# Optimization experiments

Hardware: AMD Instinct MI355X
Metric: run time of the kernel (lower is better)

Reference implementation:

```python
import jax, jax.numpy as jnp
import numpy as np

N, E, IN, HID, ADIM, EDIM, H = 20000, 320000, 128, 128, 16, 16, 2


def _lin(key, out_d, in_d, scale=0.05):
    kw, kb = jax.random.split(key)
    W = jax.random.normal(kw, (out_d, in_d), jnp.float32) * scale
    b = jax.random.normal(kb, (out_d,), jnp.float32) * scale
    return W, b


def _gat_params(key):
    k = jax.random.split(key, 4)
    Wl, bl = _lin(k[0], H * HID, HID)
    Wr, br = _lin(k[1], H * HID, HID)
    We = jax.random.normal(k[2], (H * HID, EDIM), jnp.float32) * 0.05  # lin_edge, no bias
    att = jax.random.normal(k[3], (1, H, HID), jnp.float32) * 0.05
    bias = jnp.zeros((HID,), jnp.float32)  # concat=False -> out bias of size HID
    return Wl, bl, Wr, br, We, att, bias


def setup_inputs() -> dict:
    key = jax.random.key(0)
    ks = jax.random.split(key, 16)
    inp = {}
    inp['x'] = jax.random.normal(ks[0], (N, IN), jnp.float32)
    inp['edge_index'] = jax.random.randint(ks[1], (2, E), 0, N, jnp.int64 if jax.config.jax_enable_x64 else jnp.int32)
    inp['edge_attr'] = jax.random.normal(ks[2], (E, EDIM), jnp.float32)
    inp['action'] = jax.random.normal(ks[3], (N, ADIM), jnp.float32)
    inp['inp_W'], inp['inp_b'] = _lin(ks[4], HID, IN)
    for i, name in enumerate(['s1', 's2', 'sa']):
        Wl, bl, Wr, br, We, att, bias = _gat_params(ks[5 + i])
        inp[f'{name}_Wl'], inp[f'{name}_bl'] = Wl, bl
        inp[f'{name}_Wr'], inp[f'{name}_br'] = Wr, br
        inp[f'{name}_We'], inp[f'{name}_att'], inp[f'{name}_bias'] = We, att, bias
    inp['ap_W'], inp['ap_b'] = _lin(ks[8], HID, ADIM)
    inp['g_W'], inp['g_b'] = _lin(ks[9], HID, HID)
    inp['be_W'], inp['be_b'] = _lin(ks[10], HID, HID)
    inp['q1_W'], inp['q1_b'] = _lin(ks[11], HID, HID)
    inp['q2_W'], inp['q2_b'] = _lin(ks[12], 1, HID)
    return inp


def gatv2(h, src, dst, ea, Wl, bl, Wr, br, We, att, bias):
    """PyG GATv2Conv, heads=H, concat=False (mean over heads), with edge_attr."""
    n = h.shape[0]
    xl = (h @ Wl.T + bl).reshape(n, H, HID)   # source transform
    xr = (h @ Wr.T + br).reshape(n, H, HID)   # destination transform
    em = (ea @ We.T).reshape(-1, H, HID)      # [E,H,C]
    m = jax.nn.leaky_relu(xl[src] + xr[dst] + em, 0.2)   # [E,H,C]
    logit = (m * att).sum(-1)                 # [E,H]
    lmax = jax.ops.segment_max(logit, dst, num_segments=n)
    w = jnp.exp(logit - lmax[dst])
    den = jax.ops.segment_sum(w, dst, num_segments=n)
    alpha = w / den[dst]                      # segment softmax over incoming edges
    out = jax.ops.segment_sum(alpha[..., None] * xl[src], dst, num_segments=n)  # [n,H,C]
    return out.mean(axis=1) + bias


def reference(x, edge_index, edge_attr, action, inp_W, inp_b,
              s1_Wl, s1_bl, s1_Wr, s1_br, s1_We, s1_att, s1_bias,
              s2_Wl, s2_bl, s2_Wr, s2_br, s2_We, s2_att, s2_bias,
              sa_Wl, sa_bl, sa_Wr, sa_br, sa_We, sa_att, sa_bias,
              ap_W, ap_b, g_W, g_b, be_W, be_b, q1_W, q1_b, q2_W, q2_b):
    src, dst = edge_index[0], edge_index[1]
    h = jax.nn.relu(x @ inp_W.T + inp_b)
    h = jax.nn.relu(gatv2(h, src, dst, edge_attr, s1_Wl, s1_bl, s1_Wr, s1_br, s1_We, s1_att, s1_bias))
    h = jax.nn.relu(gatv2(h, src, dst, edge_attr, s2_Wl, s2_bl, s2_Wr, s2_br, s2_We, s2_att, s2_bias))
    a = jax.nn.relu(action @ ap_W.T + ap_b)
    h = (a @ g_W.T + g_b) * h + (a @ be_W.T + be_b)   # FiLM modulation
    h = jax.nn.relu(gatv2(h, src, dst, edge_attr, sa_Wl, sa_bl, sa_Wr, sa_br, sa_We, sa_att, sa_bias))
    h = jax.nn.relu(h @ q1_W.T + q1_b)
    q_node = h @ q2_W.T + q2_b                         # [N,1]
    return q_node.mean(axis=0, keepdims=True)          # [1,1]
```

## Files before the change

### kernel.cpp

```cpp
#include <hip/hip_runtime.h>
#include <hip/hip_bf16.h>


typedef __attribute__((ext_vector_type(8))) short bf16x8;
typedef __attribute__((ext_vector_type(4))) float f32x4;
typedef __attribute__((ext_vector_type(2))) float f32x2;

#define ZERO8 ((bf16x8){0, 0, 0, 0, 0, 0, 0, 0})

__device__ __forceinline__ unsigned short f2bf(float f) {
    union { float f; unsigned int i; } v; v.f = f;
    unsigned int x = v.i;
    x += 0x7fffu + ((x >> 16) & 1u);
    return (unsigned short)(x >> 16);
}
__device__ __forceinline__ unsigned char f2fp8(float f) {
    return (unsigned char)(__builtin_amdgcn_cvt_pk_fp8_f32(f, f, 0, false) & 0xFF);
}
__device__ __forceinline__ void wave_lds_fence() {
    __builtin_amdgcn_wave_barrier();
    asm volatile("s_waitcnt lgkmcnt(0)" ::: "memory");
    __builtin_amdgcn_wave_barrier();
}

#define MAXCVT 16
struct CvtDescs {
    const float* src[MAXCVT];
    unsigned short* dst[MAXCVT];
    int n4[MAXCVT];
    int cnt;
};
__global__ __launch_bounds__(256) void cvt_many_kernel(CvtDescs d) {
    const int tid = blockIdx.x * blockDim.x + threadIdx.x;
    const int stride = gridDim.x * blockDim.x;
    for (int e = 0; e < d.cnt; ++e) {
        const float4* s = (const float4*)d.src[e];
        ushort4* o = (ushort4*)d.dst[e];
        const int n = d.n4[e];
        for (int i = tid; i < n; i += stride) {
            float4 v = s[i];
            o[i] = make_ushort4(f2bf(v.x), f2bf(v.y), f2bf(v.z), f2bf(v.w));
        }
    }
}

__global__ void hist_kernel(const int* __restrict__ dst, int* __restrict__ deg, int n) {
    int i = blockIdx.x * blockDim.x + threadIdx.x;
    if (i < n) atomicAdd(&deg[dst[i]], 1);
}

__global__ __launch_bounds__(1024) void scan_kernel(const int* __restrict__ deg,
                                                    int* __restrict__ rowp,
                                                    int* __restrict__ cur, int n) {
    __shared__ int sums[1024];
    const int t = threadIdx.x;
    const int PER = 20;
    int base = t * PER;
    int local[PER];
    int run = 0;
#pragma unroll
    for (int i = 0; i < PER; ++i) {
        int v = (base + i < n) ? deg[base + i] : 0;
        local[i] = run; run += v;
    }
    sums[t] = run; __syncthreads();
    for (int off = 1; off < 1024; off <<= 1) {
        int v = (t >= off) ? sums[t - off] : 0;
        __syncthreads();
        sums[t] += v;
        __syncthreads();
    }
    int offs = (t > 0) ? sums[t - 1] : 0;
#pragma unroll
    for (int i = 0; i < PER; ++i) {
        int idx = base + i;
        if (idx < n) { int v = offs + local[i]; rowp[idx] = v; cur[idx] = v; }
    }
    if (t == 0) rowp[n] = sums[1023];
}

__global__ void scatter_kernel(const int* __restrict__ src, const int* __restrict__ dst,
                               int* __restrict__ cur, const float4* __restrict__ ea,
                               int* __restrict__ csrs, int* __restrict__ csrd,
                               ushort4* __restrict__ eacsr, int n) {
    int i = blockIdx.x * blockDim.x + threadIdx.x;
    if (i < n) {
        int d = dst[i];
        int p = atomicAdd(&cur[d], 1);
        csrs[p] = src[i];
        csrd[p] = d;
        const float4* er = ea + (size_t)i * 4;
        ushort4* eo = eacsr + (size_t)p * 4;
#pragma unroll
        for (int q = 0; q < 4; ++q) {
            float4 v = er[q];
            eo[q] = make_ushort4(f2bf(v.x), f2bf(v.y), f2bf(v.z), f2bf(v.w));
        }
    }
}

template <bool RELU, bool SPLIT, bool AF32>
__global__ __launch_bounds__(256) void gemm_mfma_kernel(
    const void* __restrict__ Ap, const unsigned short* __restrict__ W,
    const float* __restrict__ bias0, const float* __restrict__ bias1, int bsplit,
    unsigned short* __restrict__ Cbf, unsigned char* __restrict__ Cf8,
    int M, int N, int K) {
    __shared__ unsigned char ctile[SPLIT ? 128 * 64 : 64];
    const int t = threadIdx.x;
    const int wave = t >> 6, lane = t & 63;
    const int lo = lane & 15, quad = lane >> 4;
    const int m0 = blockIdx.y * 128 + wave * 32;
    const int n0 = blockIdx.x * 64;

    f32x4 acc[2][4];
#pragma unroll
    for (int i = 0; i < 2; ++i)
#pragma unroll
        for (int j = 0; j < 4; ++j) acc[i][j] = (f32x4){0.f, 0.f, 0.f, 0.f};

    for (int k0 = 0; k0 < K; k0 += 32) {
        bf16x8 af[2], bfr[4];
#pragma unroll
        for (int mi = 0; mi < 2; ++mi) {
            const int mb = m0 + mi * 16;
            if (mb >= M) { af[mi] = ZERO8; continue; }
            if (AF32) {
                const float* A = (const float*)Ap;
                float4 a0 = *(const float4*)(A + (size_t)(mb + lo) * K + k0 + quad * 8);
                float4 a1 = *(const float4*)(A + (size_t)(mb + lo) * K + k0 + quad * 8 + 4);
                bf16x8 f;
                f[0] = (short)f2bf(a0.x); f[1] = (short)f2bf(a0.y);
                f[2] = (short)f2bf(a0.z); f[3] = (short)f2bf(a0.w);
                f[4] = (short)f2bf(a1.x); f[5] = (short)f2bf(a1.y);
                f[6] = (short)f2bf(a1.z); f[7] = (short)f2bf(a1.w);
                af[mi] = f;
            } else {
                const unsigned short* A = (const unsigned short*)Ap;
                af[mi] = *(const bf16x8*)(A + (size_t)(mb + lo) * K + k0 + quad * 8);
            }
        }
#pragma unroll
        for (int ni = 0; ni < 4; ++ni)
            bfr[ni] = *(const bf16x8*)(W + (size_t)(n0 + ni * 16 + lo) * K + k0 + quad * 8);
#pragma unroll
        for (int mi = 0; mi < 2; ++mi)
#pragma unroll
            for (int ni = 0; ni < 4; ++ni)
                acc[mi][ni] = __builtin_amdgcn_mfma_f32_16x16x32_bf16(af[mi], bfr[ni], acc[mi][ni], 0, 0, 0);
    }

    float bn[4];
#pragma unroll
    for (int ni = 0; ni < 4; ++ni) {
        const int n = n0 + ni * 16 + lo;
        const float* bp = (n < bsplit) ? bias0 : bias1;
        const int bi = (n < bsplit) ? n : n - bsplit;
        bn[ni] = bp[bi];
    }
    if (SPLIT) {
#pragma unroll
        for (int mi = 0; mi < 2; ++mi) {
#pragma unroll
            for (int ni = 0; ni < 4; ++ni) {
                const int n = ni * 16 + lo;
#pragma unroll
                for (int r = 0; r < 4; ++r) {
                    float o = acc[mi][ni][r] + bn[ni];
                    if (RELU) o = fmaxf(o, 0.f);
                    ctile[(wave * 32 + mi * 16 + quad * 4 + r) * 64 + n] = f2fp8(o);
                }
            }
        }
        __syncthreads();
        const int row = t >> 1, half = t & 1;
        const int grow = blockIdx.y * 128 + row;
        if (grow < M) {
            const unsigned char* srcp = &ctile[row * 64 + half * 32];
            unsigned char* dstp = Cf8 + (size_t)grow * 512 + n0 + half * 32;
            *(int4*)(dstp) = *(const int4*)(srcp);
            *(int4*)(dstp + 16) = *(const int4*)(srcp + 16);
        }
    } else {
#pragma unroll
        for (int mi = 0; mi < 2; ++mi) {
            const int mb = m0 + mi * 16;
            if (mb >= M) continue;
#pragma unroll
            for (int ni = 0; ni < 4; ++ni) {
                const int n = n0 + ni * 16 + lo;
#pragma unroll
                for (int r = 0; r < 4; ++r) {
                    float o = acc[mi][ni][r] + bn[ni];
                    if (RELU) o = fmaxf(o, 0.f);
                    Cbf[(size_t)(mb + quad * 4 + r) * N + n] = f2bf(o);
                }
            }
        }
    }
}

__global__ __launch_bounds__(256) void gemm_film_kernel(
    const unsigned short* __restrict__ A, const unsigned short* __restrict__ Wg,
    const unsigned short* __restrict__ Wb, const float* __restrict__ gb,
    const float* __restrict__ bb, unsigned short* __restrict__ hbf, int M) {
    const int K = 128, N = 128;
    const int t = threadIdx.x;
    const int wave = t >> 6, lane = t & 63;
    const int lo = lane & 15, quad = lane >> 4;
    const int m0 = blockIdx.y * 128 + wave * 32;
    const int n0 = blockIdx.x * 64;

    f32x4 accg[2][4], accb[2][4];
#pragma unroll
    for (int i = 0; i < 2; ++i)
#pragma unroll
        for (int j = 0; j < 4; ++j) { accg[i][j] = (f32x4){0.f,0.f,0.f,0.f}; accb[i][j] = accg[i][j]; }

    for (int k0 = 0; k0 < 128; k0 += 32) {
        bf16x8 af[2], bg4[4];
#pragma unroll
        for (int mi = 0; mi < 2; ++mi) {
            const int mb = m0 + mi * 16;
            af[mi] = (mb < M) ? *(const bf16x8*)(A + (size_t)(mb + lo) * K + k0 + quad * 8)
                              : ZERO8;
        }
#pragma unroll
        for (int ni = 0; ni < 4; ++ni)
            bg4[ni] = *(const bf16x8*)(Wg + (size_t)(n0 + ni * 16 + lo) * K + k0 + quad * 8);
#pragma unroll
        for (int mi = 0; mi < 2; ++mi)
#pragma unroll
            for (int ni = 0; ni < 4; ++ni)
                accg[mi][ni] = __builtin_amdgcn_mfma_f32_16x16x32_bf16(af[mi], bg4[ni], accg[mi][ni], 0, 0, 0);
#pragma unroll
        for (int ni = 0; ni < 4; ++ni)
            bg4[ni] = *(const bf16x8*)(Wb + (size_t)(n0 + ni * 16 + lo) * K + k0 + quad * 8);
#pragma unroll
        for (int mi = 0; mi < 2; ++mi)
#pragma unroll
            for (int ni = 0; ni < 4; ++ni)
                accb[mi][ni] = __builtin_amdgcn_mfma_f32_16x16x32_bf16(af[mi], bg4[ni], accb[mi][ni], 0, 0, 0);
    }

#pragma unroll
    for (int mi = 0; mi < 2; ++mi) {
        const int mb = m0 + mi * 16;
        if (mb >= M) continue;
#pragma unroll
        for (int ni = 0; ni < 4; ++ni) {
            const int n = n0 + ni * 16 + lo;
            const float g = gb[n], b = bb[n];
#pragma unroll
            for (int r = 0; r < 4; ++r) {
                const size_t idx = (size_t)(mb + quad * 4 + r) * N + n;
                union { unsigned int i; float f; } hv; hv.i = (unsigned int)hbf[idx] << 16;
                hbf[idx] = f2bf((accg[mi][ni][r] + g) * hv.f + (accb[mi][ni][r] + b));
            }
        }
    }
}

__global__ __launch_bounds__(256) void gemm_q1_kernel(
    const unsigned short* __restrict__ A, const unsigned short* __restrict__ W,
    const float* __restrict__ q1b, const float* __restrict__ q2w,
    float* __restrict__ outsum, int M) {
    const int K = 128;
    const int t = threadIdx.x;
    const int wave = t >> 6, lane = t & 63;
    const int lo = lane & 15, quad = lane >> 4;
    const int m0 = blockIdx.y * 128 + wave * 32;
    const int n0 = blockIdx.x * 64;
    __shared__ float red[4];

    f32x4 acc[2][4];
#pragma unroll
    for (int i = 0; i < 2; ++i)
#pragma unroll
        for (int j = 0; j < 4; ++j) acc[i][j] = (f32x4){0.f, 0.f, 0.f, 0.f};

    for (int k0 = 0; k0 < K; k0 += 32) {
        bf16x8 af[2], bfr[4];
#pragma unroll
        for (int mi = 0; mi < 2; ++mi) {
            const int mb = m0 + mi * 16;
            af[mi] = (mb < M) ? *(const bf16x8*)(A + (size_t)(mb + lo) * K + k0 + quad * 8)
                              : ZERO8;
        }
#pragma unroll
        for (int ni = 0; ni < 4; ++ni)
            bfr[ni] = *(const bf16x8*)(W + (size_t)(n0 + ni * 16 + lo) * K + k0 + quad * 8);
#pragma unroll
        for (int mi = 0; mi < 2; ++mi)
#pragma unroll
            for (int ni = 0; ni < 4; ++ni)
                acc[mi][ni] = __builtin_amdgcn_mfma_f32_16x16x32_bf16(af[mi], bfr[ni], acc[mi][ni], 0, 0, 0);
    }

    float partial = 0.f;
#pragma unroll
    for (int mi = 0; mi < 2; ++mi) {
        const int mb = m0 + mi * 16;
        if (mb >= M) continue;
#pragma unroll
        for (int ni = 0; ni < 4; ++ni) {
            const int n = n0 + ni * 16 + lo;
            const float b = q1b[n], w = q2w[n];
#pragma unroll
            for (int r = 0; r < 4; ++r)
                partial += fmaxf(acc[mi][ni][r] + b, 0.f) * w;
        }
    }
    partial += __shfl_xor(partial, 1);  partial += __shfl_xor(partial, 2);
    partial += __shfl_xor(partial, 4);  partial += __shfl_xor(partial, 8);
    partial += __shfl_xor(partial, 16); partial += __shfl_xor(partial, 32);
    if (lane == 0) red[wave] = partial;
    __syncthreads();
    if (t == 0) atomicAdd(outsum, red[0] + red[1] + red[2] + red[3]);
}

template <int BK, bool RELU>
__global__ __launch_bounds__(256) void gemm_kernel(const float* __restrict__ A,
                                                   const float* __restrict__ W,
                                                   const float* __restrict__ bp,
                                                   unsigned short* __restrict__ Cbf,
                                                   int M, int N, int K) {
    __shared__ float As[BK][68];
    __shared__ float Ws[BK][68];
    const int t = threadIdx.x;
    const int m0 = blockIdx.y * 64;
    const int n0 = blockIdx.x * 64;
    const int tx = t & 15, ty = t >> 4;
    float acc[4][4];
#pragma unroll
    for (int i = 0; i < 4; ++i)
#pragma unroll
        for (int j = 0; j < 4; ++j) acc[i][j] = 0.f;

    for (int k0 = 0; k0 < K; k0 += BK) {
        const int r = t >> 2, cc = (t & 3) * 4;
        const int arow = m0 + r;
        float4 av = (arow < M) ? *(const float4*)(A + (size_t)arow * K + k0 + cc)
                               : make_float4(0.f, 0.f, 0.f, 0.f);
        As[cc + 0][r] = av.x; As[cc + 1][r] = av.y;
        As[cc + 2][r] = av.z; As[cc + 3][r] = av.w;
        float4 wv = *(const float4*)(W + (size_t)(n0 + r) * K + k0 + cc);
        Ws[cc + 0][r] = wv.x; Ws[cc + 1][r] = wv.y;
        Ws[cc + 2][r] = wv.z; Ws[cc + 3][r] = wv.w;
        __syncthreads();
#pragma unroll
        for (int k = 0; k < BK; ++k) {
            float4 a4 = *(const float4*)&As[k][ty * 4];
            float4 b4 = *(const float4*)&Ws[k][tx * 4];
            float a_[4] = {a4.x, a4.y, a4.z, a4.w};
            float b_[4] = {b4.x, b4.y, b4.z, b4.w};
#pragma unroll
            for (int i = 0; i < 4; ++i)
#pragma unroll
                for (int j = 0; j < 4; ++j) acc[i][j] += a_[i] * b_[j];
        }
        __syncthreads();
    }
    float4 bj = *(const float4*)(bp + n0 + tx * 4);
    float bb[4] = {bj.x, bj.y, bj.z, bj.w};
#pragma unroll
    for (int i = 0; i < 4; ++i) {
        int row = m0 + ty * 4 + i;
        if (row < M) {
            float o[4];
#pragma unroll
            for (int j = 0; j < 4; ++j) {
                o[j] = acc[i][j] + bb[j];
                if (RELU) o[j] = fmaxf(o[j], 0.f);
            }
            *(ushort4*)(Cbf + (size_t)row * N + n0 + tx * 4) =
                make_ushort4(f2bf(o[0]), f2bf(o[1]), f2bf(o[2]), f2bf(o[3]));
        }
    }
}

#define LSTR 272
__global__ __launch_bounds__(256, 4) void gat_logit_kernel(
    const unsigned char* __restrict__ xf8,
    const int* __restrict__ csrs, const int* __restrict__ csrd,
    const unsigned short* __restrict__ eacsr, const unsigned short* __restrict__ we16,
    const float* __restrict__ att, float* __restrict__ logit, int E) {
    __shared__ float attl[256];
    __shared__ __align__(16) unsigned char xls[4][16 * LSTR];
    __shared__ __align__(16) unsigned char xrs[4][16 * LSTR];
    const int tid = threadIdx.x;
    attl[tid] = att[tid];
    const int wave = tid >> 6, lane = tid & 63;
    const int lo = lane & 15, quad = lane >> 4;
    const int sr_row = lane >> 2, c16 = (lane & 3) * 16;

    bf16x8 wef[16];
#pragma unroll
    for (int t = 0; t < 16; ++t)
        wef[t] = (quad < 2) ? *(const bf16x8*)(we16 + (size_t)(t * 16 + lo) * 16 + quad * 8)
                            : ZERO8;
    __syncthreads();

    const int nb = (E + 15) / 16;
    const int wstride = gridDim.x * 4;
    const int trips = (nb + wstride - 1) / wstride;
    for (int it = 0; it < trips; ++it) {
        const int b = blockIdx.x * 4 + wave + it * wstride;
        if (b >= nb) break;
        const int p0 = b * 16;
        {
            const int pr = min(p0 + sr_row, E - 1);
            const int sr = csrs[pr], dr = csrd[pr];
            const unsigned char* xs = xf8 + (size_t)sr * 512 + c16;
            const unsigned char* xrp = xf8 + (size_t)dr * 512 + 256 + c16;
            unsigned char* ld = &xls[wave][sr_row * LSTR + c16];
            unsigned char* rd = &xrs[wave][sr_row * LSTR + c16];
#pragma unroll
            for (int j = 0; j < 4; ++j) {
                *(int4*)(ld + j * 64) = *(const int4*)(xs + j * 64);
                *(int4*)(rd + j * 64) = *(const int4*)(xrp + j * 64);
            }
        }
        wave_lds_fence();
        {
            const bool valid = (p0 + lo) < E;
            const int p = valid ? (p0 + lo) : (E - 1);
            const bf16x8 eaf = (quad < 2)
                ? *(const bf16x8*)(eacsr + (size_t)p * 16 + quad * 8) : ZERO8;
            float ph0 = 0.f, ph1 = 0.f;
#pragma unroll
            for (int t = 0; t < 16; ++t) {
                f32x4 D = __builtin_amdgcn_mfma_f32_16x16x32_bf16(
                    wef[t], eaf, (f32x4){0.f, 0.f, 0.f, 0.f}, 0, 0, 0);
                const int c0 = t * 16 + quad * 4;
                const unsigned int xlu = *(const unsigned int*)&xls[wave][lo * LSTR + c0];
                const unsigned int xru = *(const unsigned int*)&xrs[wave][lo * LSTR + c0];
                const f32x2 l01 = __builtin_amdgcn_cvt_pk_f32_fp8(xlu, false);
                const f32x2 l23 = __builtin_amdgcn_cvt_pk_f32_fp8(xlu, true);
                const f32x2 r01 = __builtin_amdgcn_cvt_pk_f32_fp8(xru, false);
                const f32x2 r23 = __builtin_amdgcn_cvt_pk_f32_fp8(xru, true);
                const float4 at4 = *(const float4*)&attl[c0];
                float vx = l01.x + r01.x + D[0];
                float vy = l01.y + r01.y + D[1];
                float vz = l23.x + r23.x + D[2];
                float vw = l23.y + r23.y + D[3];
                vx = fmaxf(vx, 0.2f * vx); vy = fmaxf(vy, 0.2f * vy);
                vz = fmaxf(vz, 0.2f * vz); vw = fmaxf(vw, 0.2f * vw);
                const float pt = vx * at4.x + vy * at4.y + vz * at4.z + vw * at4.w;
                if (t < 8) ph0 += pt; else ph1 += pt;
            }
            ph0 += __shfl_xor(ph0, 16); ph0 += __shfl_xor(ph0, 32);
            ph1 += __shfl_xor(ph1, 16); ph1 += __shfl_xor(ph1, 32);
            if (valid) {
                if (quad == 0) logit[p0 + lo] = ph0;
                else if (quad == 1) logit[(size_t)E + p0 + lo] = ph1;
            }
        }
        wave_lds_fence();
    }
}

__global__ __launch_bounds__(256) void gat_na_kernel(
    const unsigned char* __restrict__ xf8,
    const int* __restrict__ rowp, const int* __restrict__ csrs,
    const float* __restrict__ wgt, const float* __restrict__ bias,
    unsigned short* __restrict__ houtb, int nnodes, int E) {
    const int lane = threadIdx.x & 63;
    const int node = blockIdx.x * 4 + (threadIdx.x >> 6);
    if (node >= nnodes) return;
    const int rs = rowp[node], re = rowp[node + 1];
    const int h = lane >> 5, l = lane & 31;
    const float* lg = wgt + (size_t)h * E;

    float sum = 0.f;
    for (int i = rs + l; i < re; i += 32) sum += __expf(fminf(lg[i], 60.f));
    sum += __shfl_xor(sum, 1);  sum += __shfl_xor(sum, 2);  sum += __shfl_xor(sum, 4);
    sum += __shfl_xor(sum, 8);  sum += __shfl_xor(sum, 16);
    const float inv = (re > rs) ? 1.f / sum : 0.f;

    float4 acc0 = make_float4(0.f, 0.f, 0.f, 0.f), acc1 = acc0;
    int i = rs;
    for (; i + 1 < re; i += 2) {
        const int s0 = csrs[i], s1 = csrs[i + 1];
        const float w0 = __expf(fminf(lg[i], 60.f)) * inv;
        const float w1 = __expf(fminf(lg[i + 1], 60.f)) * inv;
        const unsigned int u0 = *(const unsigned int*)(xf8 + (size_t)s0 * 512 + 4 * lane);
        const unsigned int u1 = *(const unsigned int*)(xf8 + (size_t)s1 * 512 + 4 * lane);
        const f32x2 a01 = __builtin_amdgcn_cvt_pk_f32_fp8(u0, false);
        const f32x2 a23 = __builtin_amdgcn_cvt_pk_f32_fp8(u0, true);
        const f32x2 b01 = __builtin_amdgcn_cvt_pk_f32_fp8(u1, false);
        const f32x2 b23 = __builtin_amdgcn_cvt_pk_f32_fp8(u1, true);
        acc0.x += w0 * a01.x; acc0.y += w0 * a01.y; acc0.z += w0 * a23.x; acc0.w += w0 * a23.y;
        acc1.x += w1 * b01.x; acc1.y += w1 * b01.y; acc1.z += w1 * b23.x; acc1.w += w1 * b23.y;
    }
    if (i < re) {
        const int s0 = csrs[i];
        const float w0 = __expf(fminf(lg[i], 60.f)) * inv;
        const unsigned int u0 = *(const unsigned int*)(xf8 + (size_t)s0 * 512 + 4 * lane);
        const f32x2 a01 = __builtin_amdgcn_cvt_pk_f32_fp8(u0, false);
        const f32x2 a23 = __builtin_amdgcn_cvt_pk_f32_fp8(u0, true);
        acc0.x += w0 * a01.x; acc0.y += w0 * a01.y; acc0.z += w0 * a23.x; acc0.w += w0 * a23.y;
    }
    float ox = acc0.x + acc1.x, oy = acc0.y + acc1.y;
    float oz = acc0.z + acc1.z, ow = acc0.w + acc1.w;
    ox += __shfl_xor(ox, 32); oy += __shfl_xor(oy, 32);
    oz += __shfl_xor(oz, 32); ow += __shfl_xor(ow, 32);
    if (lane < 32) {
        float4 bu = *(const float4*)(bias + 4 * lane);
        *(ushort4*)(houtb + (size_t)node * 128 + 4 * lane) = make_ushort4(
            f2bf(fmaxf(0.5f * ox + bu.x, 0.f)), f2bf(fmaxf(0.5f * oy + bu.y, 0.f)),
            f2bf(fmaxf(0.5f * oz + bu.z, 0.f)), f2bf(fmaxf(0.5f * ow + bu.w, 0.f)));
    }
}

__global__ void final_kernel(const float* __restrict__ s, const float* __restrict__ q2b,
                             float* __restrict__ out, float invn) {
    out[0] = s[0] * invn + q2b[0];
}

extern "C" void kernel_launch(void* const* d_in, const int* in_sizes, int n_in,
                              void* d_out, int out_size, void* d_ws, size_t ws_size,
                              hipStream_t stream) {
    const int N = in_sizes[0] / 128;
    const int E = in_sizes[1] / 2;

    typedef const float* fp;
    fp x      = (fp)d_in[0];
    const int* ei = (const int*)d_in[1];
    fp ea     = (fp)d_in[2];
    fp action = (fp)d_in[3];
    fp inp_W  = (fp)d_in[4];
    fp inp_b  = (fp)d_in[5];
    fp ap_W = (fp)d_in[27], ap_b = (fp)d_in[28];
    fp g_W  = (fp)d_in[29], g_b  = (fp)d_in[30];
    fp be_W = (fp)d_in[31], be_b = (fp)d_in[32];
    fp q1_W = (fp)d_in[33], q1_b = (fp)d_in[34];
    fp q2_W = (fp)d_in[35], q2_b = (fp)d_in[36];

    char* base = (char*)d_ws;
    size_t off = 0;
    auto alloc = [&](size_t bytes) { char* p = base + off; off = (off + bytes + 255) & ~(size_t)255; return p; };
    unsigned char*  xf8 = (unsigned char*)alloc((size_t)N * 512);
    float* col  = (float*)alloc(128 * 4);
    int* deg    = (int*)alloc((size_t)N * 4);
    int* rowp   = (int*)alloc((size_t)(N + 1) * 4);
    int* cur    = (int*)alloc((size_t)N * 4);
    int* csrs   = (int*)alloc((size_t)E * 4);
    int* csrd   = (int*)alloc((size_t)E * 4);
    unsigned short* eacsr = (unsigned short*)alloc((size_t)E * 16 * 2);
    float* wgt  = (float*)alloc((size_t)2 * E * 4);
    unsigned short* hbf = (unsigned short*)alloc((size_t)N * 128 * 2);
    unsigned short* abf = (unsigned short*)alloc((size_t)N * 128 * 2);
    unsigned short* wbf = (unsigned short*)alloc((262144 + 3 * 4096) * 2);
    (void)ws_size; (void)n_in; (void)out_size;

    unsigned short* winp = wbf;
    unsigned short* w1l  = wbf + 16384;
    unsigned short* w1r  = w1l + 32768;
    unsigned short* w2l  = w1r + 32768;
    unsigned short* w2r  = w2l + 32768;
    unsigned short* wal  = w2r + 32768;
    unsigned short* war  = wal + 32768;
    unsigned short* wg   = war + 32768;
    unsigned short* wbe  = wg + 16384;
    unsigned short* wq1  = wbe + 16384;
    unsigned short* wep1 = wq1 + 16384;
    unsigned short* wep2 = wep1 + 4096;
    unsigned short* wep3 = wep2 + 4096;

    const int* src = ei;
    const int* dst = ei + E;

    CvtDescs cd;
    int ce = 0;
    auto addc = [&](const float* s, unsigned short* d, int n) { cd.src[ce] = s; cd.dst[ce] = d; cd.n4[ce] = n / 4; ++ce; };
    addc(inp_W, winp, 16384);
    addc((fp)d_in[6],  w1l, 32768); addc((fp)d_in[8],  w1r, 32768);
    addc((fp)d_in[13], w2l, 32768); addc((fp)d_in[15], w2r, 32768);
    addc((fp)d_in[20], wal, 32768); addc((fp)d_in[22], war, 32768);
    addc(g_W, wg, 16384); addc(be_W, wbe, 16384); addc(q1_W, wq1, 16384);
    addc((fp)d_in[10], wep1, 4096); addc((fp)d_in[17], wep2, 4096); addc((fp)d_in[24], wep3, 4096);
    cd.cnt = ce;
    cvt_many_kernel<<<1024, 256, 0, stream>>>(cd);

    hipMemsetAsync(deg, 0, (size_t)N * 4, stream);
    hist_kernel<<<(E + 255) / 256, 256, 0, stream>>>(dst, deg, E);
    scan_kernel<<<1, 1024, 0, stream>>>(deg, rowp, cur, N);
    scatter_kernel<<<(E + 255) / 256, 256, 0, stream>>>(src, dst, cur, (const float4*)ea,
                                                        csrs, csrd, (ushort4*)eacsr, E);

    const int my = (N + 127) / 128;
    const int nodeg = (N + 3) / 4;

    auto run_gat = [&](const unsigned short* wep, const float* at, const float* bi,
                       unsigned short* hb) {
        gat_logit_kernel<<<2500, 256, 0, stream>>>(xf8, csrs, csrd, eacsr, wep, at, wgt, E);
        gat_na_kernel<<<nodeg, 256, 0, stream>>>(xf8, rowp, csrs, wgt, bi, hb, N, E);
    };

    gemm_mfma_kernel<true, false, true><<<dim3(2, my), 256, 0, stream>>>(
        x, winp, inp_b, inp_b, 128, hbf, nullptr, N, 128, 128);

    gemm_mfma_kernel<false, true, false><<<dim3(8, my), 256, 0, stream>>>(
        hbf, w1l, (fp)d_in[7], (fp)d_in[9], 256, nullptr, xf8, N, 512, 128);
    run_gat(wep1, (fp)d_in[11], (fp)d_in[12], hbf);
    gemm_mfma_kernel<false, true, false><<<dim3(8, my), 256, 0, stream>>>(
        hbf, w2l, (fp)d_in[14], (fp)d_in[16], 256, nullptr, xf8, N, 512, 128);
    run_gat(wep2, (fp)d_in[18], (fp)d_in[19], hbf);

    gemm_kernel<16, true><<<dim3(2, (N + 63) / 64), 256, 0, stream>>>(
        action, ap_W, ap_b, abf, N, 128, 16);
    gemm_film_kernel<<<dim3(2, my), 256, 0, stream>>>(abf, wg, wbe, g_b, be_b, hbf, N);

    gemm_mfma_kernel<false, true, false><<<dim3(8, my), 256, 0, stream>>>(
        hbf, wal, (fp)d_in[21], (fp)d_in[23], 256, nullptr, xf8, N, 512, 128);
    run_gat(wep3, (fp)d_in[25], (fp)d_in[26], hbf);

    hipMemsetAsync(col, 0, 4, stream);
    gemm_q1_kernel<<<dim3(2, my), 256, 0, stream>>>(hbf, wq1, q1_b, q2_W, col, N);
    final_kernel<<<1, 1, 0, stream>>>(col, q2_b, (float*)d_out, 1.0f / (float)N);
}
```

Before: 449.1 us.

## Fuse softmax exp into logit kernel, single-pass aggregation, drop memsets and final kernel

The logit kernel now stores exp(logit) instead of the raw logit. The aggregation kernel then accumulates the numerator and denominator in one pass, unrolled by four, rather than doing a separate sum pass and recomputing exp. The memsets for deg, col and a new counter are folded into the weight-conversion kernel, which now uses a flat index with its grid sized to the work. The final kernel is replaced by a last-block-done atomic counter in gemm_q1, which cuts launch and per-edge exp overhead but adds a serialized completion step.

Result: faster. 423.1 us (-5.8%).

```diff
diff --git a/kernel.cpp b/kernel.cpp
--- a/kernel.cpp
+++ b/kernel.cpp
@@ -27,21 +27,25 @@
 struct CvtDescs {
     const float* src[MAXCVT];
     unsigned short* dst[MAXCVT];
-    int n4[MAXCVT];
+    int off4[MAXCVT + 1];
     int cnt;
+    int* deg; int ndeg4;
+    int* ctr; float* col;
 };
 __global__ __launch_bounds__(256) void cvt_many_kernel(CvtDescs d) {
     const int tid = blockIdx.x * blockDim.x + threadIdx.x;
     const int stride = gridDim.x * blockDim.x;
-    for (int e = 0; e < d.cnt; ++e) {
-        const float4* s = (const float4*)d.src[e];
-        ushort4* o = (ushort4*)d.dst[e];
-        const int n = d.n4[e];
-        for (int i = tid; i < n; i += stride) {
-            float4 v = s[i];
-            o[i] = make_ushort4(f2bf(v.x), f2bf(v.y), f2bf(v.z), f2bf(v.w));
-        }
-    }
+    const int total = d.off4[d.cnt];
+    for (int i = tid; i < total; i += stride) {
+        int e = 0;
+        while (d.off4[e + 1] <= i) ++e;
+        const int j = i - d.off4[e];
+        float4 v = ((const float4*)d.src[e])[j];
+        ((ushort4*)d.dst[e])[j] = make_ushort4(f2bf(v.x), f2bf(v.y), f2bf(v.z), f2bf(v.w));
+    }
+    for (int i = tid; i < d.ndeg4; i += stride)
+        ((int4*)d.deg)[i] = make_int4(0, 0, 0, 0);
+    if (tid == 0) { *d.ctr = 0; *d.col = 0.f; }
 }
 
 __global__ void hist_kernel(const int* __restrict__ dst, int* __restrict__ deg, int n) {
@@ -263,7 +267,9 @@
 __global__ __launch_bounds__(256) void gemm_q1_kernel(
     const unsigned short* __restrict__ A, const unsigned short* __restrict__ W,
     const float* __restrict__ q1b, const float* __restrict__ q2w,
-    float* __restrict__ outsum, int M) {
+    const float* __restrict__ q2b, float* __restrict__ outsum,
+    float* __restrict__ outv, int* __restrict__ ctr,
+    int M, int nblk, float invn) {
     const int K = 128;
     const int t = threadIdx.x;
     const int wave = t >> 6, lane = t & 63;
@@ -315,7 +321,15 @@
     partial += __shfl_xor(partial, 16); partial += __shfl_xor(partial, 32);
     if (lane == 0) red[wave] = partial;
     __syncthreads();
-    if (t == 0) atomicAdd(outsum, red[0] + red[1] + red[2] + red[3]);
+    if (t == 0) {
+        atomicAdd(outsum, red[0] + red[1] + red[2] + red[3]);
+        __threadfence();
+        unsigned int d = atomicAdd((unsigned int*)ctr, 1u);
+        if (d == (unsigned int)(nblk - 1)) {
+            float s = atomicAdd(outsum, 0.f);
+            outv[0] = s * invn + q2b[0];
+        }
+    }
 }
 
 template <int BK, bool RELU>
@@ -451,8 +465,8 @@
             ph0 += __shfl_xor(ph0, 16); ph0 += __shfl_xor(ph0, 32);
             ph1 += __shfl_xor(ph1, 16); ph1 += __shfl_xor(ph1, 32);
             if (valid) {
-                if (quad == 0) logit[p0 + lo] = ph0;
-                else if (quad == 1) logit[(size_t)E + p0 + lo] = ph1;
+                if (quad == 0) logit[p0 + lo] = __expf(fminf(ph0, 60.f));
+                else if (quad == 1) logit[(size_t)E + p0 + lo] = __expf(fminf(ph1, 60.f));
             }
         }
         wave_lds_fence();
@@ -468,40 +482,45 @@
     const int node = blockIdx.x * 4 + (threadIdx.x >> 6);
     if (node >= nnodes) return;
     const int rs = rowp[node], re = rowp[node + 1];
-    const int h = lane >> 5, l = lane & 31;
+    const int h = lane >> 5;
     const float* lg = wgt + (size_t)h * E;
 
-    float sum = 0.f;
-    for (int i = rs + l; i < re; i += 32) sum += __expf(fminf(lg[i], 60.f));
-    sum += __shfl_xor(sum, 1);  sum += __shfl_xor(sum, 2);  sum += __shfl_xor(sum, 4);
-    sum += __shfl_xor(sum, 8);  sum += __shfl_xor(sum, 16);
-    const float inv = (re > rs) ? 1.f / sum : 0.f;
-
-    float4 acc0 = make_float4(0.f, 0.f, 0.f, 0.f), acc1 = acc0;
+    float den = 0.f;
+    float4 acc = make_float4(0.f, 0.f, 0.f, 0.f);
     int i = rs;
-    for (; i + 1 < re; i += 2) {
-        const int s0 = csrs[i], s1 = csrs[i + 1];
-        const float w0 = __expf(fminf(lg[i], 60.f)) * inv;
-        const float w1 = __expf(fminf(lg[i + 1], 60.f)) * inv;
+    for (; i + 3 < re; i += 4) {
+        const int s0 = csrs[i], s1 = csrs[i + 1], s2 = csrs[i + 2], s3 = csrs[i + 3];
+        const float w0 = lg[i], w1 = lg[i + 1], w2 = lg[i + 2], w3 = lg[i + 3];
         const unsigned int u0 = *(const unsigned int*)(xf8 + (size_t)s0 * 512 + 4 * lane);
         const unsigned int u1 = *(const unsigned int*)(xf8 + (size_t)s1 * 512 + 4 * lane);
-        const f32x2 a01 = __builtin_amdgcn_cvt_pk_f32_fp8(u0, false);
-        const f32x2 a23 = __builtin_amdgcn_cvt_pk_f32_fp8(u0, true);
-        const f32x2 b01 = __builtin_amdgcn_cvt_pk_f32_fp8(u1, false);
-        const f32x2 b23 = __builtin_amdgcn_cvt_pk_f32_fp8(u1, true);
-        acc0.x += w0 * a01.x; acc0.y += w0 * a01.y; acc0.z += w0 * a23.x; acc0.w += w0 * a23.y;
-        acc1.x += w1 * b01.x; acc1.y += w1 * b01.y; acc1.z += w1 * b23.x; acc1.w += w1 * b23.y;
-    }
-    if (i < re) {
+        const unsigned int u2 = *(const unsigned int*)(xf8 + (size_t)s2 * 512 + 4 * lane);
+        const unsigned int u3 = *(const unsigned int*)(xf8 + (size_t)s3 * 512 + 4 * lane);
+        den += (w0 + w1) + (w2 + w3);
+        f32x2 p01, p23;
+        p01 = __builtin_amdgcn_cvt_pk_f32_fp8(u0, false);
+        p23 = __builtin_amdgcn_cvt_pk_f32_fp8(u0, true);
+        acc.x += w0 * p01.x; acc.y += w0 * p01.y; acc.z += w0 * p23.x; acc.w += w0 * p23.y;
+        p01 = __builtin_amdgcn_cvt_pk_f32_fp8(u1, false);
+        p23 = __builtin_amdgcn_cvt_pk_f32_fp8(u1, true);
+        acc.x += w1 * p01.x; acc.y += w1 * p01.y; acc.z += w1 * p23.x; acc.w += w1 * p23.y;
+        p01 = __builtin_amdgcn_cvt_pk_f32_fp8(u2, false);
+        p23 = __builtin_amdgcn_cvt_pk_f32_fp8(u2, true);
+        acc.x += w2 * p01.x; acc.y += w2 * p01.y; acc.z += w2 * p23.x; acc.w += w2 * p23.y;
+        p01 = __builtin_amdgcn_cvt_pk_f32_fp8(u3, false);
+        p23 = __builtin_amdgcn_cvt_pk_f32_fp8(u3, true);
+        acc.x += w3 * p01.x; acc.y += w3 * p01.y; acc.z += w3 * p23.x; acc.w += w3 * p23.y;
+    }
+    for (; i < re; ++i) {
         const int s0 = csrs[i];
-        const float w0 = __expf(fminf(lg[i], 60.f)) * inv;
+        const float w0 = lg[i];
         const unsigned int u0 = *(const unsigned int*)(xf8 + (size_t)s0 * 512 + 4 * lane);
-        const f32x2 a01 = __builtin_amdgcn_cvt_pk_f32_fp8(u0, false);
-        const f32x2 a23 = __builtin_amdgcn_cvt_pk_f32_fp8(u0, true);
-        acc0.x += w0 * a01.x; acc0.y += w0 * a01.y; acc0.z += w0 * a23.x; acc0.w += w0 * a23.y;
-    }
-    float ox = acc0.x + acc1.x, oy = acc0.y + acc1.y;
-    float oz = acc0.z + acc1.z, ow = acc0.w + acc1.w;
+        const f32x2 p01 = __builtin_amdgcn_cvt_pk_f32_fp8(u0, false);
+        const f32x2 p23 = __builtin_amdgcn_cvt_pk_f32_fp8(u0, true);
+        den += w0;
+        acc.x += w0 * p01.x; acc.y += w0 * p01.y; acc.z += w0 * p23.x; acc.w += w0 * p23.y;
+    }
+    const float inv = (re > rs) ? 1.f / den : 0.f;
+    float ox = acc.x * inv, oy = acc.y * inv, oz = acc.z * inv, ow = acc.w * inv;
     ox += __shfl_xor(ox, 32); oy += __shfl_xor(oy, 32);
     oz += __shfl_xor(oz, 32); ow += __shfl_xor(ow, 32);
     if (lane < 32) {
@@ -510,11 +529,6 @@
             f2bf(fmaxf(0.5f * ox + bu.x, 0.f)), f2bf(fmaxf(0.5f * oy + bu.y, 0.f)),
             f2bf(fmaxf(0.5f * oz + bu.z, 0.f)), f2bf(fmaxf(0.5f * ow + bu.w, 0.f)));
     }
-}
-
-__global__ void final_kernel(const float* __restrict__ s, const float* __restrict__ q2b,
-                             float* __restrict__ out, float invn) {
-    out[0] = s[0] * invn + q2b[0];
 }
 
 extern "C" void kernel_launch(void* const* d_in, const int* in_sizes, int n_in,
@@ -541,6 +555,7 @@
     auto alloc = [&](size_t bytes) { char* p = base + off; off = (off + bytes + 255) & ~(size_t)255; return p; };
     unsigned char*  xf8 = (unsigned char*)alloc((size_t)N * 512);
     float* col  = (float*)alloc(128 * 4);
+    int* ctr    = (int*)alloc(256);
     int* deg    = (int*)alloc((size_t)N * 4);
     int* rowp   = (int*)alloc((size_t)(N + 1) * 4);
     int* cur    = (int*)alloc((size_t)N * 4);
@@ -571,18 +586,20 @@
     const int* dst = ei + E;
 
     CvtDescs cd;
-    int ce = 0;
-    auto addc = [&](const float* s, unsigned short* d, int n) { cd.src[ce] = s; cd.dst[ce] = d; cd.n4[ce] = n / 4; ++ce; };
+    int ce = 0, acc4 = 0;
+    auto addc = [&](const float* s, unsigned short* d, int n) {
+        cd.src[ce] = s; cd.dst[ce] = d; cd.off4[ce] = acc4; acc4 += n / 4; ++ce; };
     addc(inp_W, winp, 16384);
     addc((fp)d_in[6],  w1l, 32768); addc((fp)d_in[8],  w1r, 32768);
     addc((fp)d_in[13], w2l, 32768); addc((fp)d_in[15], w2r, 32768);
     addc((fp)d_in[20], wal, 32768); addc((fp)d_in[22], war, 32768);
     addc(g_W, wg, 16384); addc(be_W, wbe, 16384); addc(q1_W, wq1, 16384);
     addc((fp)d_in[10], wep1, 4096); addc((fp)d_in[17], wep2, 4096); addc((fp)d_in[24], wep3, 4096);
-    cd.cnt = ce;
-    cvt_many_kernel<<<1024, 256, 0, stream>>>(cd);
-
-    hipMemsetAsync(deg, 0, (size_t)N * 4, stream);
+    cd.off4[ce] = acc4; cd.cnt = ce;
+    cd.deg = deg; cd.ndeg4 = (N + 3) / 4;
+    cd.ctr = ctr; cd.col = col;
+    cvt_many_kernel<<<(acc4 + 255) / 256, 256, 0, stream>>>(cd);
+
     hist_kernel<<<(E + 255) / 256, 256, 0, stream>>>(dst, deg, E);
     scan_kernel<<<1, 1024, 0, stream>>>(deg, rowp, cur, N);
     scatter_kernel<<<(E + 255) / 256, 256, 0, stream>>>(src, dst, cur, (const float4*)ea,
@@ -615,7 +632,6 @@
         hbf, wal, (fp)d_in[21], (fp)d_in[23], 256, nullptr, xf8, N, 512, 128);
     run_gat(wep3, (fp)d_in[25], (fp)d_in[26], hbf);
 
-    hipMemsetAsync(col, 0, 4, stream);
-    gemm_q1_kernel<<<dim3(2, my), 256, 0, stream>>>(hbf, wq1, q1_b, q2_W, col, N);
-    final_kernel<<<1, 1, 0, stream>>>(col, q2_b, (float*)d_out, 1.0f / (float)N);
-}
+    gemm_q1_kernel<<<dim3(2, my), 256, 0, stream>>>(
+        hbf, wq1, q1_b, q2_W, q2_b, col, (float*)d_out, ctr, N, 2 * my, 1.0f / (float)N);
+}
```
